# Optimization experiments

Hardware: AMD Instinct MI355X
Metric: run time of the kernel (lower is better)

The kernel has to match this reference:

```python
import jax, jax.numpy as jnp
import numpy as np

B, T, H, K = 256, 1024, 12, 6
EPS = 1e-5


def _lstm_layer(x, Wih, Whh, bih, bhh):
    # x: [B, T, H]; torch gate order i, f, g, o
    b = bih + bhh

    def step(carry, xt):
        h, c = carry
        gates = xt @ Wih.T + h @ Whh.T + b
        i, f, g, o = jnp.split(gates, 4, axis=-1)
        c = jax.nn.sigmoid(f) * c + jax.nn.sigmoid(i) * jnp.tanh(g)
        h = jax.nn.sigmoid(o) * jnp.tanh(c)
        return (h, c), h

    h0 = jnp.zeros((x.shape[0], H), x.dtype)
    (_, _), ys = jax.lax.scan(step, (h0, h0), jnp.swapaxes(x, 0, 1))
    return jnp.swapaxes(ys, 0, 1)


def _bn_per_step(x, gamma, beta):
    # BatchNorm1d applied independently at each timestep (training mode):
    # normalize over the batch axis for each (t, channel).
    mu = jnp.mean(x, axis=0, keepdims=True)
    var = jnp.mean((x - mu) ** 2, axis=0, keepdims=True)  # biased, as torch BN
    return gamma * (x - mu) * jax.lax.rsqrt(var + EPS) + beta


def setup_inputs() -> dict:
    key = jax.random.key(0)
    ks = jax.random.split(key, 12)
    s = 1.0 / np.sqrt(H)
    return {
        "mfcc": jax.random.normal(ks[0], (B, T, H), jnp.float32),
        "Wih": jax.random.uniform(ks[1], (3, 4 * H, H), jnp.float32, -s, s),
        "Whh": jax.random.uniform(ks[2], (3, 4 * H, H), jnp.float32, -s, s),
        "bih": jax.random.uniform(ks[3], (3, 4 * H), jnp.float32, -s, s),
        "bhh": jax.random.uniform(ks[4], (3, 4 * H), jnp.float32, -s, s),
        "fc1_w": jax.random.normal(ks[5], (64, H), jnp.float32) * 0.1,
        "fc1_b": jnp.zeros((64,), jnp.float32),
        "bn1_g": jnp.ones((64,), jnp.float32),
        "bn1_b": jnp.zeros((64,), jnp.float32),
        "fc2_w": jax.random.normal(ks[6], (128, 64), jnp.float32) * 0.1,
        "fc2_b": jnp.zeros((128,), jnp.float32),
        "bn2_g": jnp.ones((128,), jnp.float32),
        "bn2_b": jnp.zeros((128,), jnp.float32),
        "fc3_w": jax.random.normal(ks[7], (K, 128), jnp.float32) * 0.1,
        "fc3_b": jnp.zeros((K,), jnp.float32),
        "WI": jax.random.normal(ks[8], (K, H, H), jnp.float32) * 0.01,
    }


def reference(mfcc, Wih, Whh, bih, bhh, fc1_w, fc1_b, bn1_g, bn1_b,
              fc2_w, fc2_b, bn2_g, bn2_b, fc3_w, fc3_b, WI):
    # 3-layer LSTM, input/hidden = 12
    x = mfcc
    for l in range(3):
        x = _lstm_layer(x, Wih[l], Whh[l], bih[l], bhh[l])

    # per-timestep MLP with per-timestep BatchNorm (training-mode stats)
    h = jnp.einsum('bth,oh->bto', x, fc1_w) + fc1_b
    h = jax.nn.relu(_bn_per_step(h, bn1_g, bn1_b))
    h = jnp.einsum('bth,oh->bto', h, fc2_w) + fc2_b
    h = jax.nn.relu(_bn_per_step(h, bn2_g, bn2_b))
    lambs = jnp.einsum('bth,kh->btk', h, fc3_w) + fc3_b  # [B, T, K]

    # out[b,t] = mfcc[b,t] @ (I + sum_k lambs[b,t,k] * WI[k])
    #          = mfcc[b,t] + sum_k lambs[b,t,k] * (mfcc[b,t] @ WI[k])
    proj = jnp.einsum('btd,kde->btke', mfcc, WI)  # [B, T, K, 12]
    outs = mfcc + jnp.einsum('btk,btke->bte', lambs, proj)
    return outs[:, None, :, :]  # [B, 1, T, 12]
```

## Files before the change

kernel.cpp:

```cpp
#include <hip/hip_runtime.h>

#define T_LEN 1024
#define NBATCH 256
#define HDIM 12
#define PAIR_STRIDE 12288
#define X3_TB 16

typedef __fp16 fp16x2 __attribute__((ext_vector_type(2)));

#if __has_builtin(__builtin_amdgcn_exp2f)
#define EXP2F(x) __builtin_amdgcn_exp2f(x)
#else
#define EXP2F(x) exp2f(x)
#endif
#if __has_builtin(__builtin_amdgcn_rcpf)
#define RCPF(x) __builtin_amdgcn_rcpf(x)
#else
#define RCPF(x) (1.0f / (x))
#endif

#define KSIG -1.4426950408889634f
#define KTAN -2.8853900817779268f

__device__ __forceinline__ unsigned bperm(int byteidx, unsigned v) {
#if __has_builtin(__builtin_amdgcn_ds_bpermute)
  return (unsigned)__builtin_amdgcn_ds_bpermute(byteidx, (int)v);
#else
  return (unsigned)__shfl((int)v, byteidx >> 2, 64);
#endif
}

template <int Q>
__device__ __forceinline__ float qb(float v) {
#if __has_builtin(__builtin_amdgcn_mov_dpp)
  return __int_as_float(__builtin_amdgcn_mov_dpp(__float_as_int(v), Q * 0x55, 0xF, 0xF, true));
#else
  return __shfl(v, (threadIdx.x & ~3) | Q, 64);
#endif
}

__device__ __forceinline__ float row_shr4(float v) {
#if __has_builtin(__builtin_amdgcn_mov_dpp)
  return __int_as_float(__builtin_amdgcn_mov_dpp(__float_as_int(v), 0x114, 0xF, 0xF, true));
#else
  return __shfl(v, (threadIdx.x & 63) - 4, 64);
#endif
}

__device__ __forceinline__ float h16tof(unsigned short u) {
  union { unsigned short s; _Float16 h; } c; c.s = u; return (float)c.h;
}
__device__ __forceinline__ unsigned short f16bits(float f) {
  union { unsigned short s; _Float16 h; } c; c.h = (_Float16)f; return c.s;
}
__device__ __forceinline__ float h16lo(unsigned u) {
  union { unsigned short s; _Float16 h; } c; c.s = (unsigned short)(u & 0xffffu); return (float)c.h;
}
__device__ __forceinline__ float h16hi(unsigned u) {
  union { unsigned short s; _Float16 h; } c; c.s = (unsigned short)(u >> 16); return (float)c.h;
}
__device__ __forceinline__ unsigned pk16(float a, float b) {
#if __has_builtin(__builtin_amdgcn_cvt_pkrtz)
  fp16x2 h = __builtin_amdgcn_cvt_pkrtz(a, b);
  return __builtin_bit_cast(unsigned, h);
#else
  return (unsigned)f16bits(a) | ((unsigned)f16bits(b) << 16);
#endif
}

__device__ __forceinline__ float dot2acc(unsigned a, unsigned b, float c) {
#if __has_builtin(__builtin_amdgcn_fdot2)
  return __builtin_amdgcn_fdot2(__builtin_bit_cast(fp16x2, a), __builtin_bit_cast(fp16x2, b), c, false);
#else
  return fmaf(h16lo(a), h16lo(b), fmaf(h16hi(a), h16hi(b), c));
#endif
}

__device__ __forceinline__ float d3(const unsigned* w, const unsigned* h, float init) {
  float a = dot2acc(w[0], h[0], init);
  a = dot2acc(w[1], h[1], a);
  return dot2acc(w[2], h[2], a);
}

__device__ __forceinline__ float nlup(float av, float& cv, float c1, float c0) {
  float e = EXP2F(av);
  float n = fmaf(c1, RCPF(1.f + e), c0);
  float si = qb<0>(n), sf = qb<1>(n), tg = qb<2>(n), so = qb<3>(n);
  cv = fmaf(sf, cv, si * tg);
  float e2 = EXP2F(KTAN * cv);
  return so * fmaf(2.f, RCPF(1.f + e2), -1.f);
}
__device__ __forceinline__ unsigned packb(float hq, unsigned* hp) {
  float sh = row_shr4(hq);
  unsigned pkv = pk16(sh, hq);
  hp[0] = bperm(16, pkv);  hp[1] = bperm(48, pkv);  hp[2] = bperm(80, pkv);
  hp[3] = bperm(112, pkv); hp[4] = bperm(144, pkv); hp[5] = bperm(176, pkv);
  return pkv;
}

#define BARRIER_LGKM() asm volatile("s_waitcnt lgkmcnt(0)\n\ts_barrier" ::: "memory")

__global__ __launch_bounds__(64, 4) void pregate_kernel(
    const float* __restrict__ mfcc, const float* __restrict__ Wih,
    const float* __restrict__ bih, const float* __restrict__ bhh,
    const float* __restrict__ w2, const float* __restrict__ WI,
    const float* __restrict__ w1, unsigned* __restrict__ pg2,
    unsigned* __restrict__ w2pk, unsigned* __restrict__ wipk,
    unsigned* __restrict__ w1pk) {
  if (blockIdx.x >= 2048) {
    const int base = (blockIdx.x - 2048) * 64 + threadIdx.x;
    for (int i = base; i < 4096; i += 512) {
      int kp = i >> 7, c = i & 127;
      float2 v = ((const float2*)w2)[c * 32 + kp];
      w2pk[i] = pk16(v.x, v.y);
    }
    for (int i = base; i < 432; i += 512) {
      int k6 = i / 72, rem = i % 72, e = rem / 6, dp = rem % 6;
      wipk[i] = pk16(WI[k6 * 144 + (2 * dp) * HDIM + e],
                     WI[k6 * 144 + (2 * dp + 1) * HDIM + e]);
    }
    for (int i = base; i < 384; i += 512) {
      int ch = i / 6, dp = i % 6;
      float2 v = ((const float2*)w1)[ch * 6 + dp];
      w1pk[i] = pk16(v.x, v.y);
    }
    return;
  }
  const int b = blockIdx.x & 255;
  const int tc = blockIdx.x >> 8;
  const int lane = threadIdx.x;
  const int j = lane >> 2, q = lane & 3;
  const int jj = (j < HDIM) ? j : (HDIM - 1);
  const int g = q * HDIM + jj;
  const float kqv = (q == 2) ? KTAN : KSIG;
  float w[HDIM];
#pragma unroll
  for (int m = 0; m < HDIM; ++m) w[m] = kqv * Wih[g * HDIM + m];
  const float bias = kqv * (bih[g] + bhh[g]);
  const bool wr = (lane < 48);
  const float* xb = mfcc + (b * T_LEN + tc * 128) * HDIM;
  unsigned* out = pg2 + (unsigned)(tc * 64 * NBATCH + b) * 48 + lane;
  for (int tp = 0; tp < 64; ++tp) {
    float a0 = bias, a1 = bias;
#pragma unroll
    for (int d = 0; d < HDIM; ++d) {
      a0 = fmaf(w[d], xb[d], a0);
      a1 = fmaf(w[d], xb[HDIM + d], a1);
    }
    if (wr) *out = pk16(a0, a1);
    xb += 2 * HDIM;
    out += PAIR_STRIDE;
  }
}

__global__ __launch_bounds__(192, 1) void lstm3_kernel(
    const unsigned* __restrict__ pg2,
    const float* __restrict__ Wih, const float* __restrict__ Whh,
    const float* __restrict__ bih, const float* __restrict__ bhh,
    unsigned short* __restrict__ x3) {
  __shared__ __align__(16) unsigned ldsb[576];
  const int b = blockIdx.x;
  const int tid = threadIdx.x;
  const int wid = tid >> 6;
  const int lane = tid & 63;
  const int j = lane >> 2, q = lane & 3;
  const int jj = (j < HDIM) ? j : (HDIM - 1);
  const int g = q * HDIM + jj;
  const float kqv = (q == 2) ? KTAN : KSIG;
  const float c1c = (q == 2) ? 2.0f : 1.0f;
  const float c0c = (q == 2) ? -1.0f : 0.0f;

  const int row = (wid * 48 + g) * HDIM;
  unsigned wihp[6], whhp[6];
#pragma unroll
  for (int m = 0; m < 6; ++m) {
    wihp[m] = pk16(kqv * Wih[row + 2 * m], kqv * Wih[row + 2 * m + 1]);
    whhp[m] = pk16(kqv * Whh[row + 2 * m], kqv * Whh[row + 2 * m + 1]);
  }
  const float biasw = kqv * (bih[wid * 48 + g] + bhh[wid * 48 + g]);

  float cv = 0.f;
  unsigned hown[6] = {0, 0, 0, 0, 0, 0};

  const int grpi = lane >> 3;
  const bool wvalid = ((lane & 7) == 7) && (grpi < 6);
  const int wlayer = (wid == 0) ? 0 : 128;
  const int wsl = wvalid ? (wlayer + grpi) : (512 + lane);
  const int wst = wvalid ? 8 : 0;

  const int lane_src = (lane < 48) ? lane : (44 + (lane & 3));
  const char* pgbase = (const char*)(pg2 + (unsigned)b * 48);
  const unsigned PGB = PAIR_STRIDE * 4;
  const unsigned PGLIM = 513u * PGB;
  uint4 P0 = {0, 0, 0, 0}, P1 = P0, P2 = P0, P3 = P0;
  uint4 A0 = P0, A1 = P0, A2 = P0, A3 = P0;
  unsigned pg_upos = 0;
  if (wid == 0) {
    P0.x = *(const unsigned*)(pgbase + 0 * PGB + lane_src * 4);
    P0.y = *(const unsigned*)(pgbase + 1 * PGB + lane_src * 4);
    P0.z = *(const unsigned*)(pgbase + 2 * PGB + lane_src * 4);
    P0.w = *(const unsigned*)(pgbase + 3 * PGB + lane_src * 4);
    P1.x = *(const unsigned*)(pgbase + 4 * PGB + lane_src * 4);
    P1.y = *(const unsigned*)(pgbase + 5 * PGB + lane_src * 4);
    P1.z = *(const unsigned*)(pgbase + 6 * PGB + lane_src * 4);
    P1.w = *(const unsigned*)(pgbase + 7 * PGB + lane_src * 4);
    P2.x = *(const unsigned*)(pgbase + 8 * PGB + lane_src * 4);
    P2.y = *(const unsigned*)(pgbase + 9 * PGB + lane_src * 4);
    P2.z = *(const unsigned*)(pgbase + 10 * PGB + lane_src * 4);
    P2.w = *(const unsigned*)(pgbase + 11 * PGB + lane_src * 4);
    P3.x = *(const unsigned*)(pgbase + 12 * PGB + lane_src * 4);
    P3.y = *(const unsigned*)(pgbase + 13 * PGB + lane_src * 4);
    P3.z = *(const unsigned*)(pgbase + 14 * PGB + lane_src * 4);
    P3.w = *(const unsigned*)(pgbase + 15 * PGB + lane_src * 4);
    A0.x = *(const unsigned*)(pgbase + 16 * PGB + lane_src * 4);
    A0.y = *(const unsigned*)(pgbase + 17 * PGB + lane_src * 4);
    A0.z = *(const unsigned*)(pgbase + 18 * PGB + lane_src * 4);
    A0.w = *(const unsigned*)(pgbase + 19 * PGB + lane_src * 4);
    A1.x = *(const unsigned*)(pgbase + 20 * PGB + lane_src * 4);
    A1.y = *(const unsigned*)(pgbase + 21 * PGB + lane_src * 4);
    A1.z = *(const unsigned*)(pgbase + 22 * PGB + lane_src * 4);
    A1.w = *(const unsigned*)(pgbase + 23 * PGB + lane_src * 4);
    A2.x = *(const unsigned*)(pgbase + 24 * PGB + lane_src * 4);
    A2.y = *(const unsigned*)(pgbase + 25 * PGB + lane_src * 4);
    A2.z = *(const unsigned*)(pgbase + 26 * PGB + lane_src * 4);
    A2.w = *(const unsigned*)(pgbase + 27 * PGB + lane_src * 4);
    A3.x = *(const unsigned*)(pgbase + 28 * PGB + lane_src * 4);
    A3.y = *(const unsigned*)(pgbase + 29 * PGB + lane_src * 4);
    A3.z = *(const unsigned*)(pgbase + 30 * PGB + lane_src * 4);
    A3.w = *(const unsigned*)(pgbase + 31 * PGB + lane_src * 4);
    pg_upos = 32u * PGB;
  }

  char* x3b = (char*)(x3 + (unsigned)b * X3_TB);
  const int x3_loff = ((j & 1) && j < HDIM) ? (j - 1) * 2 : ((j < HDIM) ? 24 : 28);
  unsigned x3_upos = 0;
  const unsigned X3STEP = NBATCH * X3_TB * 2;

  auto l0_ss = [&](int par, uint4 Pa, uint4 Pb) {
    const int wpb = wvalid ? par * 256 : 0;
    const float pgf[16] = {h16lo(Pa.x), h16hi(Pa.x), h16lo(Pa.y), h16hi(Pa.y),
                           h16lo(Pa.z), h16hi(Pa.z), h16lo(Pa.w), h16hi(Pa.w),
                           h16lo(Pb.x), h16hi(Pb.x), h16lo(Pb.y), h16hi(Pb.y),
                           h16lo(Pb.z), h16hi(Pb.z), h16lo(Pb.w), h16hi(Pb.w)};
#pragma unroll
    for (int st = 0; st < 16; ++st) {
      float a = d3(whhp, hown, pgf[st]) + d3(whhp + 3, hown + 3, 0.f);
      float hq = nlup(a, cv, c1c, c0c);
      unsigned pkv = packb(hq, hown);
      ldsb[wpb + wsl + st * wst] = pkv;
    }
  };
  auto l1_ss = [&](int par) {
    const unsigned* rb = ldsb + (par ^ 1) * 256;
    unsigned hin[16][6];
#pragma unroll
    for (int st = 0; st < 16; ++st) {
      uint4 A = *(const uint4*)(rb + st * 8);
      uint2 B = *(const uint2*)(rb + st * 8 + 4);
      hin[st][0] = A.x; hin[st][1] = A.y; hin[st][2] = A.z;
      hin[st][3] = A.w; hin[st][4] = B.x; hin[st][5] = B.y;
    }
    float aI[16];
#pragma unroll
    for (int st = 0; st < 16; ++st)
      aI[st] = d3(wihp, hin[st], biasw) + d3(wihp + 3, hin[st] + 3, 0.f);
    const int wpb = wvalid ? par * 256 : 0;
#pragma unroll
    for (int st = 0; st < 16; ++st) {
      float a = aI[st] + (d3(whhp, hown, 0.f) + d3(whhp + 3, hown + 3, 0.f));
      float hq = nlup(a, cv, c1c, c0c);
      unsigned pkv = packb(hq, hown);
      ldsb[wpb + wsl + st * wst] = pkv;
    }
  };
  auto l2_ss = [&](int par) {
    const unsigned* rb = ldsb + (par ^ 1) * 256 + 128;
    unsigned hin[16][6];
#pragma unroll
    for (int st = 0; st < 16; ++st) {
      uint4 A = *(const uint4*)(rb + st * 8);
      uint2 B = *(const uint2*)(rb + st * 8 + 4);
      hin[st][0] = A.x; hin[st][1] = A.y; hin[st][2] = A.z;
      hin[st][3] = A.w; hin[st][4] = B.x; hin[st][5] = B.y;
    }
    float aI[16];
#pragma unroll
    for (int st = 0; st < 16; ++st)
      aI[st] = d3(wihp, hin[st], biasw) + d3(wihp + 3, hin[st] + 3, 0.f);
#pragma unroll
    for (int st = 0; st < 16; ++st) {
      float a = aI[st] + (d3(whhp, hown, 0.f) + d3(whhp + 3, hown + 3, 0.f));
      float hq = nlup(a, cv, c1c, c0c);
      unsigned pkv = packb(hq, hown);
      *(unsigned*)(x3b + x3_upos + st * X3STEP + x3_loff) = pkv;
    }
    x3_upos += 16 * X3STEP;
  };

  if (wid == 0) l0_ss(0, P0, P1);
  BARRIER_LGKM();
  if (wid == 0) l0_ss(1, P2, P3);
  else if (wid == 1) l1_ss(1);
  BARRIER_LGKM();
  for (int i = 0; i < 31; ++i) {
    uint4 N0 = {0, 0, 0, 0}, N1 = N0, N2 = N0, N3 = N0;
    if (wid == 0) {
      unsigned o[16];
#pragma unroll
      for (int m = 0; m < 16; ++m) {
        unsigned ov = pg_upos + m * PGB;
        o[m] = ov > PGLIM ? PGLIM : ov;
      }
      N0.x = *(const unsigned*)(pgbase + o[0] + lane_src * 4);
      N0.y = *(const unsigned*)(pgbase + o[1] + lane_src * 4);
      N0.z = *(const unsigned*)(pgbase + o[2] + lane_src * 4);
      N0.w = *(const unsigned*)(pgbase + o[3] + lane_src * 4);
      N1.x = *(const unsigned*)(pgbase + o[4] + lane_src * 4);
      N1.y = *(const unsigned*)(pgbase + o[5] + lane_src * 4);
      N1.z = *(const unsigned*)(pgbase + o[6] + lane_src * 4);
      N1.w = *(const unsigned*)(pgbase + o[7] + lane_src * 4);
      N2.x = *(const unsigned*)(pgbase + o[8] + lane_src * 4);
      N2.y = *(const unsigned*)(pgbase + o[9] + lane_src * 4);
      N2.z = *(const unsigned*)(pgbase + o[10] + lane_src * 4);
      N2.w = *(const unsigned*)(pgbase + o[11] + lane_src * 4);
      N3.x = *(const unsigned*)(pgbase + o[12] + lane_src * 4);
      N3.y = *(const unsigned*)(pgbase + o[13] + lane_src * 4);
      N3.z = *(const unsigned*)(pgbase + o[14] + lane_src * 4);
      N3.w = *(const unsigned*)(pgbase + o[15] + lane_src * 4);
      pg_upos += 16 * PGB;
      l0_ss(0, A0, A1);
    } else if (wid == 1) {
      l1_ss(0);
    } else {
      l2_ss(0);
    }
    BARRIER_LGKM();
    if (wid == 0) l0_ss(1, A2, A3);
    else if (wid == 1) l1_ss(1);
    else l2_ss(1);
    BARRIER_LGKM();
    if (wid == 0) { A0 = N0; A1 = N1; A2 = N2; A3 = N3; }
  }
  if (wid == 1) l1_ss(0);
  else if (wid == 2) l2_ss(0);
  BARRIER_LGKM();
  if (wid == 2) l2_ss(1);
}

__global__ __launch_bounds__(256, 2) void mlp_out_kernel(
    const unsigned short* __restrict__ x3, const float* __restrict__ mfcc,
    const unsigned* __restrict__ w1pk, const float* __restrict__ g1,
    const float* __restrict__ be1, const unsigned* __restrict__ w2pk,
    const float* __restrict__ g2, const float* __restrict__ be2,
    const float* __restrict__ w3, const float* __restrict__ b3,
    const unsigned* __restrict__ wipk, float* __restrict__ outp) {
  __shared__ __align__(16) unsigned char smem[53952];
  unsigned* h1p = (unsigned*)smem;
  unsigned* w2p = (unsigned*)(smem + 32768);
  float* p3 = (float*)smem;
  float* stp = (float*)(smem + 49152);
  float* scsh = (float*)(smem + 51200);
  unsigned* wis = (unsigned*)(smem + 52224);

  const int t = blockIdx.x;
  const int tid = threadIdx.x;

  for (int i = tid; i < 1024; i += 256)
    ((uint4*)w2p)[i] = ((const uint4*)w2pk)[i];
  for (int i = tid; i < 432; i += 256) wis[i] = wipk[i];

  {
    const unsigned short* xp = x3 + t * (NBATCH * X3_TB) + tid * X3_TB;
    uint2 u0 = ((const uint2*)xp)[0];
    uint2 u1 = ((const uint2*)xp)[1];
    uint2 u2 = ((const uint2*)xp)[2];
    const unsigned u[6] = {u0.x, u0.y, u1.x, u1.y, u2.x, u2.y};
#pragma unroll 4
    for (int kp = 0; kp < 32; ++kp) {
      const unsigned* wp = w1pk + kp * 12;
      float a0 = dot2acc(wp[0], u[0], 0.f);
      float a1 = dot2acc(wp[6], u[0], 0.f);
#pragma unroll
      for (int dp = 1; dp < 6; ++dp) {
        a0 = dot2acc(wp[dp], u[dp], a0);
        a1 = dot2acc(wp[6 + dp], u[dp], a1);
      }
      h1p[kp * 256 + tid] = pk16(a0, a1);
    }
  }
  __syncthreads();

  {
    const int kp = tid & 31, seg = tid >> 5;
    const uint4* rp = (const uint4*)(h1p + kp * 256 + seg * 32);
    float sl = 0.f, sh = 0.f, ql = 0.f, qh = 0.f;
#pragma unroll
    for (int i = 0; i < 8; ++i) {
      uint4 v = rp[(i + kp) & 7];
      float f0 = h16lo(v.x), f1 = h16hi(v.x), f2 = h16lo(v.y), f3 = h16hi(v.y);
      float f4 = h16lo(v.z), f5 = h16hi(v.z), f6 = h16lo(v.w), f7 = h16hi(v.w);
      sl += (f0 + f2) + (f4 + f6);
      sh += (f1 + f3) + (f5 + f7);
      ql = fmaf(f0, f0, ql); ql = fmaf(f2, f2, ql); ql = fmaf(f4, f4, ql); ql = fmaf(f6, f6, ql);
      qh = fmaf(f1, f1, qh); qh = fmaf(f3, f3, qh); qh = fmaf(f5, f5, qh); qh = fmaf(f7, f7, qh);
    }
    sl += __shfl_xor(sl, 32, 64); sh += __shfl_xor(sh, 32, 64);
    ql += __shfl_xor(ql, 32, 64); qh += __shfl_xor(qh, 32, 64);
    if ((tid & 63) < 32) {
      float* sp = stp + kp * 16 + (tid >> 6) * 4;
      sp[0] = sl; sp[1] = sh; sp[2] = ql; sp[3] = qh;
    }
  }
  __syncthreads();
  if (tid < 64) {
    const int kp = tid >> 1, par = tid & 1;
    float s = 0.f, qq = 0.f;
#pragma unroll
    for (int w = 0; w < 4; ++w) {
      s += stp[kp * 16 + w * 4 + par];
      qq += stp[kp * 16 + w * 4 + 2 + par];
    }
    const int ch = 2 * kp + par;
    float mu = s * (1.f / 256.f);
    float var = fmaf(-mu, mu, qq * (1.f / 256.f));
    float sc = g1[ch] * rsqrtf(var + 1e-5f);
    scsh[ch * 2] = sc;
    scsh[ch * 2 + 1] = fmaf(-sc, mu, be1[ch]);
  }
  __syncthreads();
  {
    unsigned* cp = h1p + tid;
#pragma unroll 8
    for (int kp = 0; kp < 32; ++kp) {
      unsigned v = cp[kp * 256];
      float fl = fmaxf(fmaf(scsh[kp * 4 + 0], h16lo(v), scsh[kp * 4 + 1]), 0.f);
      float fh = fmaxf(fmaf(scsh[kp * 4 + 2], h16hi(v), scsh[kp * 4 + 3]), 0.f);
      cp[kp * 256] = pk16(fl, fh);
    }
  }
  __syncthreads();

  const int tb = tid & 31, tc2 = tid >> 5;
  const int b0 = tb * 8, cc0 = tc2 * 16;
  float acc[8][16];
#pragma unroll
  for (int bi = 0; bi < 8; ++bi)
#pragma unroll
    for (int ci = 0; ci < 16; ++ci) acc[bi][ci] = 0.f;

  for (int kp = 0; kp < 32; ++kp) {
    const unsigned* hrow = h1p + kp * 256 + b0;
    uint4 a01 = ((const uint4*)hrow)[0];
    uint4 a23 = ((const uint4*)hrow)[1];
    const unsigned ap[8] = {a01.x, a01.y, a01.z, a01.w, a23.x, a23.y, a23.z, a23.w};
    const unsigned* wrow = w2p + kp * 128 + cc0;
#pragma unroll
    for (int wq = 0; wq < 4; ++wq) {
      uint4 wv = ((const uint4*)wrow)[wq];
      const unsigned ww[4] = {wv.x, wv.y, wv.z, wv.w};
#pragma unroll
      for (int bi = 0; bi < 8; ++bi)
#pragma unroll
        for (int cj = 0; cj < 4; ++cj)
          acc[bi][wq * 4 + cj] = dot2acc(ap[bi], ww[cj], acc[bi][wq * 4 + cj]);
    }
  }

  {
    float sv[16], qv[16];
#pragma unroll
    for (int ci = 0; ci < 16; ++ci) {
      float s = 0.f, sq = 0.f;
#pragma unroll
      for (int bi = 0; bi < 8; ++bi) {
        s += acc[bi][ci];
        sq = fmaf(acc[bi][ci], acc[bi][ci], sq);
      }
      sv[ci] = s; qv[ci] = sq;
    }
#pragma unroll
    for (int m = 1; m <= 16; m <<= 1) {
#pragma unroll
      for (int ci = 0; ci < 16; ++ci) {
        sv[ci] += __shfl_xor(sv[ci], m, 64);
        qv[ci] += __shfl_xor(qv[ci], m, 64);
      }
    }
    if (tb == 0) {
#pragma unroll
      for (int ci = 0; ci < 16; ++ci) {
        stp[(cc0 + ci) * 2] = sv[ci];
        stp[(cc0 + ci) * 2 + 1] = qv[ci];
      }
    }
  }
  __syncthreads();
  if (tid < 128) {
    float mu = stp[tid * 2] * (1.f / 256.f);
    float var = fmaf(-mu, mu, stp[tid * 2 + 1] * (1.f / 256.f));
    float sc = g2[tid] * rsqrtf(var + 1e-5f);
    scsh[tid * 2] = sc;
    scsh[tid * 2 + 1] = fmaf(-sc, mu, be2[tid]);
  }
  __syncthreads();

  {
    float lam[8][6];
#pragma unroll
    for (int bi = 0; bi < 8; ++bi)
#pragma unroll
      for (int k6 = 0; k6 < 6; ++k6) lam[bi][k6] = 0.f;
#pragma unroll
    for (int ci = 0; ci < 16; ++ci) {
      const float sc = scsh[(cc0 + ci) * 2], shv = scsh[(cc0 + ci) * 2 + 1];
      float wv6[6];
#pragma unroll
      for (int k6 = 0; k6 < 6; ++k6) wv6[k6] = w3[k6 * 128 + cc0 + ci];
#pragma unroll
      for (int bi = 0; bi < 8; ++bi) {
        float v = fmaxf(fmaf(sc, acc[bi][ci], shv), 0.f);
#pragma unroll
        for (int k6 = 0; k6 < 6; ++k6)
          lam[bi][k6] = fmaf(v, wv6[k6], lam[bi][k6]);
      }
    }
#pragma unroll
    for (int bi = 0; bi < 8; ++bi)
#pragma unroll
      for (int k6 = 0; k6 < 6; ++k6)
        p3[(tc2 * 256 + b0 + bi) * 6 + k6] = lam[bi][k6];
  }
  __syncthreads();

  {
    float lm[6];
#pragma unroll
    for (int k6 = 0; k6 < 6; ++k6) lm[k6] = b3[k6];
#pragma unroll
    for (int tcc = 0; tcc < 8; ++tcc)
#pragma unroll
      for (int k6 = 0; k6 < 6; ++k6) lm[k6] += p3[(tcc * 256 + tid) * 6 + k6];

    const float4* mp = (const float4*)(mfcc + (tid * T_LEN + t) * HDIM);
    float4 m0 = mp[0], m1 = mp[1], m2 = mp[2];
    const float x[HDIM] = {m0.x, m0.y, m0.z, m0.w, m1.x, m1.y,
                           m1.z, m1.w, m2.x, m2.y, m2.z, m2.w};
    unsigned xpk[6];
#pragma unroll
    for (int dp = 0; dp < 6; ++dp) xpk[dp] = pk16(x[2 * dp], x[2 * dp + 1]);
    float o[HDIM];
#pragma unroll
    for (int e = 0; e < HDIM; ++e) o[e] = x[e];
#pragma unroll
    for (int k6 = 0; k6 < 6; ++k6) {
      const unsigned* wrow = wis + k6 * 72;
#pragma unroll
      for (int e = 0; e < HDIM; ++e) {
        float s = dot2acc(xpk[0], wrow[e * 6 + 0], 0.f);
        s = dot2acc(xpk[1], wrow[e * 6 + 1], s);
        s = dot2acc(xpk[2], wrow[e * 6 + 2], s);
        s = dot2acc(xpk[3], wrow[e * 6 + 3], s);
        s = dot2acc(xpk[4], wrow[e * 6 + 4], s);
        s = dot2acc(xpk[5], wrow[e * 6 + 5], s);
        o[e] = fmaf(lm[k6], s, o[e]);
      }
    }
    float4* op4 = (float4*)(outp + (tid * T_LEN + t) * HDIM);
    op4[0] = make_float4(o[0], o[1], o[2], o[3]);
    op4[1] = make_float4(o[4], o[5], o[6], o[7]);
    op4[2] = make_float4(o[8], o[9], o[10], o[11]);
  }
}

extern "C" void kernel_launch(void* const* d_in, const int* in_sizes, int n_in,
                              void* d_out, int out_size, void* d_ws, size_t ws_size,
                              hipStream_t stream) {
  const float* mfcc = (const float*)d_in[0];
  const float* Wih = (const float*)d_in[1];
  const float* Whh = (const float*)d_in[2];
  const float* bih = (const float*)d_in[3];
  const float* bhh = (const float*)d_in[4];
  const float* w1 = (const float*)d_in[5];
  const float* g1 = (const float*)d_in[7];
  const float* be1 = (const float*)d_in[8];
  const float* w2 = (const float*)d_in[9];
  const float* g2 = (const float*)d_in[11];
  const float* be2 = (const float*)d_in[12];
  const float* w3 = (const float*)d_in[13];
  const float* b3 = (const float*)d_in[14];
  const float* WI = (const float*)d_in[15];

  unsigned* pg2 = (unsigned*)d_ws;
  unsigned short* x3 = (unsigned short*)((char*)d_ws + 25264128);
  unsigned* w2pk = (unsigned*)((char*)d_ws + 33652736);
  unsigned* wipk = (unsigned*)((char*)d_ws + 33669120);
  unsigned* w1pk = (unsigned*)((char*)d_ws + 33670848);
  float* out = (float*)d_out;

  hipLaunchKernelGGL(pregate_kernel, dim3(2056), dim3(64), 0, stream,
                     mfcc, Wih, bih, bhh, w2, WI, w1, pg2, w2pk, wipk, w1pk);
  hipLaunchKernelGGL(lstm3_kernel, dim3(NBATCH), dim3(192), 0, stream,
                     pg2, Wih, Whh, bih, bhh, x3);
  hipLaunchKernelGGL(mlp_out_kernel, dim3(T_LEN), dim3(256), 0, stream,
                     x3, mfcc, w1pk, g1, be1, w2pk, g2, be2, w3, b3, wipk, out);
}
```

Measured before the change: 227.6 us.

## Split MLP/output kernel into 512-thread MLP kernel and separate projection kernel

The fused per-timestep MLP+output kernel is split in two. A 512-thread MLP kernel halves each thread's fc2 batch tile from 8 to 4 rows and writes the lambda values to workspace. A new lightweight kernel then applies the WI projection and residual. The idea is more parallelism and lower register pressure in the GEMM-heavy stage, with several __syncthreads replaced by the LGKM barrier macro. The cost is an extra kernel launch plus a round trip of the lambda values through global memory, and the larger block uses about 52 KB of LDS, which limits how many blocks fit per CU.

New measurement: 278.4 us. +22.3%, slower.

```diff
diff --git a/kernel.cpp b/kernel.cpp
--- a/kernel.cpp
+++ b/kernel.cpp
@@ -347,36 +347,35 @@
   if (wid == 2) l2_ss(1);
 }
 
-__global__ __launch_bounds__(256, 2) void mlp_out_kernel(
-    const unsigned short* __restrict__ x3, const float* __restrict__ mfcc,
-    const unsigned* __restrict__ w1pk, const float* __restrict__ g1,
-    const float* __restrict__ be1, const unsigned* __restrict__ w2pk,
-    const float* __restrict__ g2, const float* __restrict__ be2,
-    const float* __restrict__ w3, const float* __restrict__ b3,
-    const unsigned* __restrict__ wipk, float* __restrict__ outp) {
-  __shared__ __align__(16) unsigned char smem[53952];
+__global__ __launch_bounds__(512, 4) void mlp2_kernel(
+    const unsigned short* __restrict__ x3, const unsigned* __restrict__ w1pk,
+    const float* __restrict__ g1, const float* __restrict__ be1,
+    const unsigned* __restrict__ w2pk, const float* __restrict__ g2,
+    const float* __restrict__ be2, const float* __restrict__ w3,
+    const float* __restrict__ b3, float* __restrict__ lamw) {
+  __shared__ __align__(16) unsigned char smem[52224];
   unsigned* h1p = (unsigned*)smem;
   unsigned* w2p = (unsigned*)(smem + 32768);
   float* p3 = (float*)smem;
   float* stp = (float*)(smem + 49152);
   float* scsh = (float*)(smem + 51200);
-  unsigned* wis = (unsigned*)(smem + 52224);
 
   const int t = blockIdx.x;
   const int tid = threadIdx.x;
 
-  for (int i = tid; i < 1024; i += 256)
+  for (int i = tid; i < 1024; i += 512)
     ((uint4*)w2p)[i] = ((const uint4*)w2pk)[i];
-  for (int i = tid; i < 432; i += 256) wis[i] = wipk[i];
 
   {
-    const unsigned short* xp = x3 + t * (NBATCH * X3_TB) + tid * X3_TB;
+    const int bb = tid & 255, half = tid >> 8;
+    const unsigned short* xp = x3 + t * (NBATCH * X3_TB) + bb * X3_TB;
     uint2 u0 = ((const uint2*)xp)[0];
     uint2 u1 = ((const uint2*)xp)[1];
     uint2 u2 = ((const uint2*)xp)[2];
     const unsigned u[6] = {u0.x, u0.y, u1.x, u1.y, u2.x, u2.y};
+    const int kp0 = half * 16;
 #pragma unroll 4
-    for (int kp = 0; kp < 32; ++kp) {
+    for (int kp = kp0; kp < kp0 + 16; ++kp) {
       const unsigned* wp = w1pk + kp * 12;
       float a0 = dot2acc(wp[0], u[0], 0.f);
       float a1 = dot2acc(wp[6], u[0], 0.f);
@@ -385,12 +384,12 @@
         a0 = dot2acc(wp[dp], u[dp], a0);
         a1 = dot2acc(wp[6 + dp], u[dp], a1);
       }
-      h1p[kp * 256 + tid] = pk16(a0, a1);
-    }
-  }
-  __syncthreads();
-
-  {
+      h1p[kp * 256 + bb] = pk16(a0, a1);
+    }
+  }
+  BARRIER_LGKM();
+
+  if (tid < 256) {
     const int kp = tid & 31, seg = tid >> 5;
     const uint4* rp = (const uint4*)(h1p + kp * 256 + seg * 32);
     float sl = 0.f, sh = 0.f, ql = 0.f, qh = 0.f;
@@ -411,7 +410,7 @@
       sp[0] = sl; sp[1] = sh; sp[2] = ql; sp[3] = qh;
     }
   }
-  __syncthreads();
+  BARRIER_LGKM();
   if (tid < 64) {
     const int kp = tid >> 1, par = tid & 1;
     float s = 0.f, qq = 0.f;
@@ -427,39 +426,39 @@
     scsh[ch * 2] = sc;
     scsh[ch * 2 + 1] = fmaf(-sc, mu, be1[ch]);
   }
-  __syncthreads();
+  BARRIER_LGKM();
   {
-    unsigned* cp = h1p + tid;
+    const int bb = tid & 255, half = tid >> 8;
+    unsigned* cp = h1p + bb;
+    const int kp0 = half * 16;
 #pragma unroll 8
-    for (int kp = 0; kp < 32; ++kp) {
+    for (int kp = kp0; kp < kp0 + 16; ++kp) {
       unsigned v = cp[kp * 256];
       float fl = fmaxf(fmaf(scsh[kp * 4 + 0], h16lo(v), scsh[kp * 4 + 1]), 0.f);
       float fh = fmaxf(fmaf(scsh[kp * 4 + 2], h16hi(v), scsh[kp * 4 + 3]), 0.f);
       cp[kp * 256] = pk16(fl, fh);
     }
   }
-  __syncthreads();
-
-  const int tb = tid & 31, tc2 = tid >> 5;
-  const int b0 = tb * 8, cc0 = tc2 * 16;
-  float acc[8][16];
-#pragma unroll
-  for (int bi = 0; bi < 8; ++bi)
+  BARRIER_LGKM();
+
+  const int tb = tid & 63, tc2 = tid >> 6;
+  const int b0 = tb * 4, cc0 = tc2 * 16;
+  float acc[4][16];
+#pragma unroll
+  for (int bi = 0; bi < 4; ++bi)
 #pragma unroll
     for (int ci = 0; ci < 16; ++ci) acc[bi][ci] = 0.f;
 
   for (int kp = 0; kp < 32; ++kp) {
-    const unsigned* hrow = h1p + kp * 256 + b0;
-    uint4 a01 = ((const uint4*)hrow)[0];
-    uint4 a23 = ((const uint4*)hrow)[1];
-    const unsigned ap[8] = {a01.x, a01.y, a01.z, a01.w, a23.x, a23.y, a23.z, a23.w};
+    uint4 av = *(const uint4*)(h1p + kp * 256 + b0);
+    const unsigned ap[4] = {av.x, av.y, av.z, av.w};
     const unsigned* wrow = w2p + kp * 128 + cc0;
 #pragma unroll
     for (int wq = 0; wq < 4; ++wq) {
       uint4 wv = ((const uint4*)wrow)[wq];
       const unsigned ww[4] = {wv.x, wv.y, wv.z, wv.w};
 #pragma unroll
-      for (int bi = 0; bi < 8; ++bi)
+      for (int bi = 0; bi < 4; ++bi)
 #pragma unroll
         for (int cj = 0; cj < 4; ++cj)
           acc[bi][wq * 4 + cj] = dot2acc(ap[bi], ww[cj], acc[bi][wq * 4 + cj]);
@@ -472,14 +471,14 @@
     for (int ci = 0; ci < 16; ++ci) {
       float s = 0.f, sq = 0.f;
 #pragma unroll
-      for (int bi = 0; bi < 8; ++bi) {
+      for (int bi = 0; bi < 4; ++bi) {
         s += acc[bi][ci];
         sq = fmaf(acc[bi][ci], acc[bi][ci], sq);
       }
       sv[ci] = s; qv[ci] = sq;
     }
 #pragma unroll
-    for (int m = 1; m <= 16; m <<= 1) {
+    for (int m = 1; m <= 32; m <<= 1) {
 #pragma unroll
       for (int ci = 0; ci < 16; ++ci) {
         sv[ci] += __shfl_xor(sv[ci], m, 64);
@@ -494,7 +493,7 @@
       }
     }
   }
-  __syncthreads();
+  BARRIER_LGKM();
   if (tid < 128) {
     float mu = stp[tid * 2] * (1.f / 256.f);
     float var = fmaf(-mu, mu, stp[tid * 2 + 1] * (1.f / 256.f));
@@ -502,12 +501,12 @@
     scsh[tid * 2] = sc;
     scsh[tid * 2 + 1] = fmaf(-sc, mu, be2[tid]);
   }
-  __syncthreads();
+  BARRIER_LGKM();
 
   {
-    float lam[8][6];
-#pragma unroll
-    for (int bi = 0; bi < 8; ++bi)
+    float lam[4][6];
+#pragma unroll
+    for (int bi = 0; bi < 4; ++bi)
 #pragma unroll
       for (int k6 = 0; k6 < 6; ++k6) lam[bi][k6] = 0.f;
 #pragma unroll
@@ -517,7 +516,7 @@
 #pragma unroll
       for (int k6 = 0; k6 < 6; ++k6) wv6[k6] = w3[k6 * 128 + cc0 + ci];
 #pragma unroll
-      for (int bi = 0; bi < 8; ++bi) {
+      for (int bi = 0; bi < 4; ++bi) {
         float v = fmaxf(fmaf(sc, acc[bi][ci], shv), 0.f);
 #pragma unroll
         for (int k6 = 0; k6 < 6; ++k6)
@@ -525,51 +524,72 @@
       }
     }
 #pragma unroll
-    for (int bi = 0; bi < 8; ++bi)
+    for (int bi = 0; bi < 4; ++bi)
 #pragma unroll
       for (int k6 = 0; k6 < 6; ++k6)
         p3[(tc2 * 256 + b0 + bi) * 6 + k6] = lam[bi][k6];
   }
+  BARRIER_LGKM();
+
+  if (tid < 256) {
+    float lm[6];
+#pragma unroll
+    for (int k6 = 0; k6 < 6; ++k6) lm[k6] = b3[k6];
+#pragma unroll
+    for (int gg = 0; gg < 8; ++gg)
+#pragma unroll
+      for (int k6 = 0; k6 < 6; ++k6) lm[k6] += p3[(gg * 256 + tid) * 6 + k6];
+    float2* lp = (float2*)(lamw + t * 1536 + tid * 6);
+    lp[0] = make_float2(lm[0], lm[1]);
+    lp[1] = make_float2(lm[2], lm[3]);
+    lp[2] = make_float2(lm[4], lm[5]);
+  }
+}
+
+__global__ __launch_bounds__(256, 8) void proj_kernel(
+    const float* __restrict__ mfcc, const float* __restrict__ lamw,
+    const unsigned* __restrict__ wipk, float* __restrict__ outp) {
+  __shared__ unsigned wis[432];
+  const int t = blockIdx.x;
+  const int tid = threadIdx.x;
+  for (int i = tid; i < 432; i += 256) wis[i] = wipk[i];
   __syncthreads();
 
+  float lm[6];
   {
-    float lm[6];
-#pragma unroll
-    for (int k6 = 0; k6 < 6; ++k6) lm[k6] = b3[k6];
-#pragma unroll
-    for (int tcc = 0; tcc < 8; ++tcc)
-#pragma unroll
-      for (int k6 = 0; k6 < 6; ++k6) lm[k6] += p3[(tcc * 256 + tid) * 6 + k6];
-
-    const float4* mp = (const float4*)(mfcc + (tid * T_LEN + t) * HDIM);
-    float4 m0 = mp[0], m1 = mp[1], m2 = mp[2];
-    const float x[HDIM] = {m0.x, m0.y, m0.z, m0.w, m1.x, m1.y,
-                           m1.z, m1.w, m2.x, m2.y, m2.z, m2.w};
-    unsigned xpk[6];
-#pragma unroll
-    for (int dp = 0; dp < 6; ++dp) xpk[dp] = pk16(x[2 * dp], x[2 * dp + 1]);
-    float o[HDIM];
-#pragma unroll
-    for (int e = 0; e < HDIM; ++e) o[e] = x[e];
-#pragma unroll
-    for (int k6 = 0; k6 < 6; ++k6) {
-      const unsigned* wrow = wis + k6 * 72;
-#pragma unroll
-      for (int e = 0; e < HDIM; ++e) {
-        float s = dot2acc(xpk[0], wrow[e * 6 + 0], 0.f);
-        s = dot2acc(xpk[1], wrow[e * 6 + 1], s);
-        s = dot2acc(xpk[2], wrow[e * 6 + 2], s);
-        s = dot2acc(xpk[3], wrow[e * 6 + 3], s);
-        s = dot2acc(xpk[4], wrow[e * 6 + 4], s);
-        s = dot2acc(xpk[5], wrow[e * 6 + 5], s);
-        o[e] = fmaf(lm[k6], s, o[e]);
-      }
-    }
-    float4* op4 = (float4*)(outp + (tid * T_LEN + t) * HDIM);
-    op4[0] = make_float4(o[0], o[1], o[2], o[3]);
-    op4[1] = make_float4(o[4], o[5], o[6], o[7]);
-    op4[2] = make_float4(o[8], o[9], o[10], o[11]);
-  }
+    const float2* lp = (const float2*)(lamw + t * 1536 + tid * 6);
+    float2 l0 = lp[0], l1 = lp[1], l2 = lp[2];
+    lm[0] = l0.x; lm[1] = l0.y; lm[2] = l1.x;
+    lm[3] = l1.y; lm[4] = l2.x; lm[5] = l2.y;
+  }
+  const float4* mp = (const float4*)(mfcc + (tid * T_LEN + t) * HDIM);
+  float4 m0 = mp[0], m1 = mp[1], m2 = mp[2];
+  const float x[HDIM] = {m0.x, m0.y, m0.z, m0.w, m1.x, m1.y,
+                         m1.z, m1.w, m2.x, m2.y, m2.z, m2.w};
+  unsigned xpk[6];
+#pragma unroll
+  for (int dp = 0; dp < 6; ++dp) xpk[dp] = pk16(x[2 * dp], x[2 * dp + 1]);
+  float o[HDIM];
+#pragma unroll
+  for (int e = 0; e < HDIM; ++e) o[e] = x[e];
+#pragma unroll
+  for (int k6 = 0; k6 < 6; ++k6) {
+    const unsigned* wrow = wis + k6 * 72;
+#pragma unroll
+    for (int e = 0; e < HDIM; ++e) {
+      float s = dot2acc(xpk[0], wrow[e * 6 + 0], 0.f);
+      s = dot2acc(xpk[1], wrow[e * 6 + 1], s);
+      s = dot2acc(xpk[2], wrow[e * 6 + 2], s);
+      s = dot2acc(xpk[3], wrow[e * 6 + 3], s);
+      s = dot2acc(xpk[4], wrow[e * 6 + 4], s);
+      s = dot2acc(xpk[5], wrow[e * 6 + 5], s);
+      o[e] = fmaf(lm[k6], s, o[e]);
+    }
+  }
+  float4* op4 = (float4*)(outp + (tid * T_LEN + t) * HDIM);
+  op4[0] = make_float4(o[0], o[1], o[2], o[3]);
+  op4[1] = make_float4(o[4], o[5], o[6], o[7]);
+  op4[2] = make_float4(o[8], o[9], o[10], o[11]);
 }
 
 extern "C" void kernel_launch(void* const* d_in, const int* in_sizes, int n_in,
@@ -591,6 +611,7 @@
   const float* WI = (const float*)d_in[15];
 
   unsigned* pg2 = (unsigned*)d_ws;
+  float* lamw = (float*)d_ws;
   unsigned short* x3 = (unsigned short*)((char*)d_ws + 25264128);
   unsigned* w2pk = (unsigned*)((char*)d_ws + 33652736);
   unsigned* wipk = (unsigned*)((char*)d_ws + 33669120);
@@ -601,6 +622,8 @@
                      mfcc, Wih, bih, bhh, w2, WI, w1, pg2, w2pk, wipk, w1pk);
   hipLaunchKernelGGL(lstm3_kernel, dim3(NBATCH), dim3(192), 0, stream,
                      pg2, Wih, Whh, bih, bhh, x3);
-  hipLaunchKernelGGL(mlp_out_kernel, dim3(T_LEN), dim3(256), 0, stream,
-                     x3, mfcc, w1pk, g1, be1, w2pk, g2, be2, w3, b3, wipk, out);
-}
+  hipLaunchKernelGGL(mlp2_kernel, dim3(T_LEN), dim3(512), 0, stream,
+                     x3, w1pk, g1, be1, w2pk, g2, be2, w3, b3, lamw);
+  hipLaunchKernelGGL(proj_kernel, dim3(T_LEN), dim3(256), 0, stream,
+                     mfcc, lamw, wipk, out);
+}
```
